# Kernel tuning notes

Measured on AMD Instinct MI355X. Metric: run time of the kernel, lower is better.

The kernel has to match this reference:

```python
import jax, jax.numpy as jnp
import numpy as np

B, R, S, M, L = 16, 64, 128, 64, 128  # batch, regions, src_dim, message_dim, max_latent
E = R * R - R  # 4032 directed edges (all ordered pairs, no self loops)


def _edge_indices():
    s, t = np.meshgrid(np.arange(R), np.arange(R), indexing='ij')
    mask = s != t
    return s[mask].astype(np.int64), t[mask].astype(np.int64)


def setup_inputs() -> dict:
    key = jax.random.key(0)
    ks = jax.random.split(key, 8)
    src_np, tgt_np = _edge_indices()
    xav_ms = float(np.sqrt(6.0 / (M + S)))  # xavier_uniform bound for (M,S) matrices
    small = 0.02  # torch inits add_w/gain_w to zeros; use small random for non-trivial outputs
    return {
        'source': jax.random.normal(ks[0], (B, R, S), jnp.float32),
        'mean_w': jax.random.uniform(ks[1], (E, M, S), jnp.float32, -xav_ms, xav_ms),
        'mean_b': jnp.zeros((E, M), jnp.float32),
        'logstd_w': jax.random.uniform(ks[2], (E, M, S), jnp.float32, -xav_ms, xav_ms),
        'logstd_b': jnp.zeros((E, M), jnp.float32),
        'add_w': small * jax.random.normal(ks[3], (E, L, M), jnp.float32),
        'gain_w': small * jax.random.normal(ks[4], (E, L, M), jnp.float32),
        'src_idx': jnp.asarray(src_np),
        'tgt_idx': jnp.asarray(tgt_np),
        'deterministic': 1,
    }


def reference(source, mean_w, mean_b, logstd_w, logstd_b, add_w, gain_w,
              src_idx, tgt_idx, deterministic):
    B_, E_ = source.shape[0], src_idx.shape[0]
    # gather source features per edge: [B, E, S]
    src = source[:, src_idx, :]
    # per-edge grouped GEMMs
    mean = jnp.einsum('bes,ems->bem', src, mean_w) + mean_b      # [B, E, M]
    logstd = jnp.einsum('bes,ems->bem', src, logstd_w) + logstd_b
    # deterministic path: msg = mean (softplus(std) only used when sampling)
    msg = mean
    add = jnp.einsum('bem,elm->bel', msg, add_w)                  # [B, E, L]
    gain = jnp.einsum('bem,elm->bel', msg, gain_w)
    # scatter-add over target regions
    inc_add = jnp.zeros((B_, R, L), source.dtype).at[:, tgt_idx].add(add)
    inc_gain = jnp.zeros((B_, R, L), source.dtype).at[:, tgt_idx].add(gain)
    # scatter (unique flat indices) into dense [B, R, R, M] message tensors
    flat = src_idx * R + tgt_idx
    def scat(x):
        return jnp.zeros((B_, R * R, M), source.dtype).at[:, flat].set(x).reshape(B_, R, R, M)
    return inc_add, inc_gain, scat(mean), scat(logstd), scat(msg)
```

## Files before the change

### kernel.cpp

```cpp
#include <hip/hip_runtime.h>

#define BB 16
#define RR 64
#define SS 128
#define MM 64
#define LL 128
#define EE 4032

#define OUT3_OFF 262144
#define ARR_SZ   4194304

__global__ __launch_bounds__(256) void k_zero(float* __restrict__ out) {
  int tid = blockIdx.x * 256 + threadIdx.x;
  if (tid < 262144) { out[tid] = 0.0f; return; }
  int idx = tid - 262144;
  int a = idx >> 16;
  int r = idx & 65535;
  int b = r >> 12;
  int d = (r >> 6) & 63;
  int m = r & 63;
  out[OUT3_OFF + (size_t)a * ARR_SZ + (size_t)b * 262144 + d * 4160 + m] = 0.0f;
}

__global__ __launch_bounds__(256) void k_edge(
    const float* __restrict__ source,
    const float* __restrict__ mean_w,
    const float* __restrict__ mean_b,
    const float* __restrict__ logstd_w,
    const float* __restrict__ logstd_b,
    const int* __restrict__ src_idx,
    const int* __restrict__ tgt_idx,
    float* __restrict__ out)
{
  __shared__ float lds_src[BB * 132];
  __shared__ float lds_mean[BB * 64];
  __shared__ float lds_logstd[BB * 64];
  const int e = blockIdx.x;
  const int tid = threadIdx.x;
  const int sidx = src_idx[e];
  const int tidx = tgt_idx[e];

  #pragma unroll
  for (int f0 = 0; f0 < 2; ++f0) {
    int f = tid + f0 * 256;
    int b = f >> 5, s4 = f & 31;
    float4 v = *(const float4*)(source + ((size_t)b * (RR * SS) + (size_t)sidx * SS + s4 * 4));
    *(float4*)(lds_src + b * 132 + s4 * 4) = v;
  }

  const int m = tid >> 2;
  const int sq = tid & 3;

  const float* wmp = mean_w   + ((size_t)e * (MM * SS) + (size_t)m * SS) + sq * 4;
  const float* wlp = logstd_w + ((size_t)e * (MM * SS) + (size_t)m * SS) + sq * 4;

  float4 a0 = *(const float4*)(wmp + 0);
  float4 c0 = *(const float4*)(wlp + 0);
  float4 a1 = *(const float4*)(wmp + 16);
  float4 c1 = *(const float4*)(wlp + 16);

  __syncthreads();

  float accm[BB], accl[BB];
  #pragma unroll
  for (int b = 0; b < BB; ++b) { accm[b] = 0.0f; accl[b] = 0.0f; }

  #pragma unroll
  for (int k = 0; k < 8; ++k) {
    float4 a2 = {}, c2 = {};
    if (k < 6) {
      a2 = *(const float4*)(wmp + (k + 2) * 16);
      c2 = *(const float4*)(wlp + (k + 2) * 16);
    }
    const int soff = sq * 4 + k * 16;
    #pragma unroll
    for (int b = 0; b < BB; ++b) {
      float4 sv = *(const float4*)(lds_src + b * 132 + soff);
      accm[b] = fmaf(a0.x, sv.x, fmaf(a0.y, sv.y, fmaf(a0.z, sv.z, fmaf(a0.w, sv.w, accm[b]))));
      accl[b] = fmaf(c0.x, sv.x, fmaf(c0.y, sv.y, fmaf(c0.z, sv.z, fmaf(c0.w, sv.w, accl[b]))));
    }
    a0 = a1; c0 = c1; a1 = a2; c1 = c2;
  }
  #pragma unroll
  for (int b = 0; b < BB; ++b) {
    accm[b] += __shfl_xor(accm[b], 1);
    accm[b] += __shfl_xor(accm[b], 2);
    accl[b] += __shfl_xor(accl[b], 1);
    accl[b] += __shfl_xor(accl[b], 2);
  }
  const float bm = mean_b[e * MM + m];
  const float bl = logstd_b[e * MM + m];
  #pragma unroll
  for (int j = 0; j < 4; ++j) {
    int b = sq * 4 + j;
    lds_mean[b * 64 + m]   = accm[b] + bm;
    lds_logstd[b * 64 + m] = accl[b] + bl;
  }
  __syncthreads();

  float* out3 = out + OUT3_OFF;
  float* out4 = out3 + ARR_SZ;
  float* out5 = out4 + ARR_SZ;
  const size_t rowbase = (size_t)(sidx * RR + tidx) * MM;
  const int b = tid >> 4, m4 = tid & 15;
  float4 vm = *(float4*)(lds_mean + b * 64 + m4 * 4);
  float4 vl = *(float4*)(lds_logstd + b * 64 + m4 * 4);
  size_t o = (size_t)b * (RR * RR * MM) + rowbase + m4 * 4;
  *(float4*)(out3 + o) = vm;
  *(float4*)(out4 + o) = vl;
  *(float4*)(out5 + o) = vm;
}

__global__ __launch_bounds__(256) void k_inc(
    const float* __restrict__ add_w,
    const float* __restrict__ gain_w,
    float* __restrict__ out)
{
  __shared__ float lds_mean[2][BB * 64];
  const int g = blockIdx.x;
  const int tt = g / 18;
  const int r = g % 18;
  const int lh = r / 9;
  const int c = r % 9;
  const int tid = threadIdx.x;
  const int l_loc = tid >> 2;
  const int mq = tid & 3;
  const int l = lh * 64 + l_loc;
  const int b16 = tid >> 4, m4 = tid & 15;

  const float* out3 = out + OUT3_OFF;

  float acca[BB], accg[BB];
  #pragma unroll
  for (int b = 0; b < BB; ++b) { acca[b] = 0.0f; accg[b] = 0.0f; }

  float4 mv_n;
  float4 wa_n[4], wg_n[4];
  {
    const int si = c * 7;
    const int s = si + (si >= tt ? 1 : 0);
    const int e = s * 63 + (tt > s ? tt - 1 : tt);
    mv_n = *(const float4*)(out3 + ((size_t)b16 * 262144 + (size_t)(s * 64 + tt) * 64 + m4 * 4));
    const float* wa = add_w  + ((size_t)e * (LL * MM) + (size_t)l * MM + mq * 16);
    const float* wg = gain_w + ((size_t)e * (LL * MM) + (size_t)l * MM + mq * 16);
    #pragma unroll
    for (int i = 0; i < 4; ++i) {
      wa_n[i] = *(const float4*)(wa + i * 4);
      wg_n[i] = *(const float4*)(wg + i * 4);
    }
  }

  #pragma unroll
  for (int j = 0; j < 7; ++j) {
    float4 mv = mv_n;
    float4 wa_c[4], wg_c[4];
    #pragma unroll
    for (int i = 0; i < 4; ++i) { wa_c[i] = wa_n[i]; wg_c[i] = wg_n[i]; }

    *(float4*)(&lds_mean[j & 1][b16 * 64 + m4 * 4]) = mv;
    __syncthreads();

    if (j < 6) {
      const int si2 = c * 7 + j + 1;
      const int s2 = si2 + (si2 >= tt ? 1 : 0);
      const int e2 = s2 * 63 + (tt > s2 ? tt - 1 : tt);
      mv_n = *(const float4*)(out3 + ((size_t)b16 * 262144 + (size_t)(s2 * 64 + tt) * 64 + m4 * 4));
      const float* wa2 = add_w  + ((size_t)e2 * (LL * MM) + (size_t)l * MM + mq * 16);
      const float* wg2 = gain_w + ((size_t)e2 * (LL * MM) + (size_t)l * MM + mq * 16);
      #pragma unroll
      for (int i = 0; i < 4; ++i) {
        wa_n[i] = *(const float4*)(wa2 + i * 4);
        wg_n[i] = *(const float4*)(wg2 + i * 4);
      }
    }

    #pragma unroll
    for (int i = 0; i < 4; ++i) {
      float4 a  = wa_c[i];
      float4 gq = wg_c[i];
      #pragma unroll
      for (int b = 0; b < BB; ++b) {
        float4 mvv = *(const float4*)(&lds_mean[j & 1][b * 64 + mq * 16 + i * 4]);
        acca[b] = fmaf(a.x,  mvv.x, fmaf(a.y,  mvv.y, fmaf(a.z,  mvv.z, fmaf(a.w,  mvv.w, acca[b]))));
        accg[b] = fmaf(gq.x, mvv.x, fmaf(gq.y, mvv.y, fmaf(gq.z, mvv.z, fmaf(gq.w, mvv.w, accg[b]))));
      }
    }
  }
  #pragma unroll
  for (int b = 0; b < BB; ++b) {
    acca[b] += __shfl_xor(acca[b], 1);
    acca[b] += __shfl_xor(acca[b], 2);
    accg[b] += __shfl_xor(accg[b], 1);
    accg[b] += __shfl_xor(accg[b], 2);
  }
  float* inc_add  = out;
  float* inc_gain = out + 131072;
  #pragma unroll
  for (int jj = 0; jj < 4; ++jj) {
    int b = mq * 4 + jj;
    size_t o = (size_t)b * (RR * LL) + (size_t)tt * LL + l;
    atomicAdd(inc_add + o, acca[b]);
    atomicAdd(inc_gain + o, accg[b]);
  }
}

extern "C" void kernel_launch(void* const* d_in, const int* in_sizes, int n_in,
                              void* d_out, int out_size, void* d_ws, size_t ws_size,
                              hipStream_t stream) {
  const float* source   = (const float*)d_in[0];
  const float* mean_w   = (const float*)d_in[1];
  const float* mean_b   = (const float*)d_in[2];
  const float* logstd_w = (const float*)d_in[3];
  const float* logstd_b = (const float*)d_in[4];
  const float* add_w    = (const float*)d_in[5];
  const float* gain_w   = (const float*)d_in[6];
  const int*   src_idx  = (const int*)d_in[7];
  const int*   tgt_idx  = (const int*)d_in[8];
  float* out = (float*)d_out;

  k_zero<<<1792, 256, 0, stream>>>(out);
  k_edge<<<EE, 256, 0, stream>>>(source, mean_w, mean_b, logstd_w, logstd_b,
                                 src_idx, tgt_idx, out);
  k_inc<<<1152, 256, 0, stream>>>(add_w, gain_w, out);
}
```

Before: 479.1 us.

## Stream edge weights into LDS via async global_load_lds with a ring buffer

The edge kernel now loads source rows and mean/logstd weight tiles straight from global memory into LDS with global_load_lds, using a four-slot ring buffer. Explicit vmcnt waits let compute on one k-chunk overlap the loads for later chunks. This removes the register staging for weights and aims to keep more memory requests in flight. In exchange it relies on manual waitcnt counting and the per-wave LDS layout being right, and it drops the padding on the source rows, which may add LDS bank conflicts.

```diff
diff --git a/kernel.cpp b/kernel.cpp
--- a/kernel.cpp
+++ b/kernel.cpp
@@ -9,6 +9,12 @@
 
 #define OUT3_OFF 262144
 #define ARR_SZ   4194304
+
+__device__ __forceinline__ void g2l16(const float* g, const float* l) {
+  __builtin_amdgcn_global_load_lds(
+      (const __attribute__((address_space(1))) unsigned int*)g,
+      (__attribute__((address_space(3))) unsigned int*)l, 16, 0, 0);
+}
 
 __global__ __launch_bounds__(256) void k_zero(float* __restrict__ out) {
   int tid = blockIdx.x * 256 + threadIdx.x;
@@ -32,55 +38,65 @@
     const int* __restrict__ tgt_idx,
     float* __restrict__ out)
 {
-  __shared__ float lds_src[BB * 132];
-  __shared__ float lds_mean[BB * 64];
-  __shared__ float lds_logstd[BB * 64];
+  __shared__ float lds[10240];
   const int e = blockIdx.x;
   const int tid = threadIdx.x;
+  const int w = tid >> 6, lane = tid & 63;
   const int sidx = src_idx[e];
   const int tidx = tgt_idx[e];
 
-  #pragma unroll
-  for (int f0 = 0; f0 < 2; ++f0) {
-    int f = tid + f0 * 256;
-    int b = f >> 5, s4 = f & 31;
-    float4 v = *(const float4*)(source + ((size_t)b * (RR * SS) + (size_t)sidx * SS + s4 * 4));
-    *(float4*)(lds_src + b * 132 + s4 * 4) = v;
-  }
-
-  const int m = tid >> 2;
-  const int sq = tid & 3;
-
-  const float* wmp = mean_w   + ((size_t)e * (MM * SS) + (size_t)m * SS) + sq * 4;
-  const float* wlp = logstd_w + ((size_t)e * (MM * SS) + (size_t)m * SS) + sq * 4;
-
-  float4 a0 = *(const float4*)(wmp + 0);
-  float4 c0 = *(const float4*)(wlp + 0);
-  float4 a1 = *(const float4*)(wmp + 16);
-  float4 c1 = *(const float4*)(wlp + 16);
-
-  __syncthreads();
+  {
+    int f0 = tid;
+    g2l16(source + (size_t)(f0 >> 5) * (RR * SS) + (size_t)sidx * SS + (f0 & 31) * 4,
+          lds + w * 256);
+    int f1 = tid + 256;
+    g2l16(source + (size_t)(f1 >> 5) * (RR * SS) + (size_t)sidx * SS + (f1 & 31) * 4,
+          lds + 1024 + w * 256);
+  }
+  __builtin_amdgcn_sched_barrier(0);
+
+  const int row = w * 16 + (lane >> 2);
+  const int sq4 = (lane & 3) * 4;
+  const float* wmg = mean_w   + (size_t)e * (MM * SS) + (size_t)row * SS + sq4;
+  const float* wlg = logstd_w + (size_t)e * (MM * SS) + (size_t)row * SS + sq4;
+  #pragma unroll
+  for (int kk = 0; kk < 4; ++kk) {
+    g2l16(wmg + kk * 16, lds + 2048 + kk * 1024 + w * 256);
+    g2l16(wlg + kk * 16, lds + 6144 + kk * 1024 + w * 256);
+  }
+  __builtin_amdgcn_sched_barrier(0);
+
+  asm volatile("s_waitcnt vmcnt(8)" ::: "memory");
+  __builtin_amdgcn_s_barrier();
 
   float accm[BB], accl[BB];
   #pragma unroll
   for (int b = 0; b < BB; ++b) { accm[b] = 0.0f; accl[b] = 0.0f; }
 
-  #pragma unroll
-  for (int k = 0; k < 8; ++k) {
-    float4 a2 = {}, c2 = {};
-    if (k < 6) {
-      a2 = *(const float4*)(wmp + (k + 2) * 16);
-      c2 = *(const float4*)(wlp + (k + 2) * 16);
-    }
-    const int soff = sq * 4 + k * 16;
-    #pragma unroll
-    for (int b = 0; b < BB; ++b) {
-      float4 sv = *(const float4*)(lds_src + b * 132 + soff);
-      accm[b] = fmaf(a0.x, sv.x, fmaf(a0.y, sv.y, fmaf(a0.z, sv.z, fmaf(a0.w, sv.w, accm[b]))));
-      accl[b] = fmaf(c0.x, sv.x, fmaf(c0.y, sv.y, fmaf(c0.z, sv.z, fmaf(c0.w, sv.w, accl[b]))));
-    }
-    a0 = a1; c0 = c1; a1 = a2; c1 = c2;
-  }
+#define KSTEP(kk, Nwait)                                                        \
+  {                                                                             \
+    asm volatile("s_waitcnt vmcnt(" #Nwait ")" ::: "memory");                   \
+    float4 a = *(const float4*)(lds + 2048 + ((kk) & 3) * 1024 + w * 256 + lane * 4); \
+    float4 c = *(const float4*)(lds + 6144 + ((kk) & 3) * 1024 + w * 256 + lane * 4); \
+    const int soff = sq4 + (kk) * 16;                                           \
+    _Pragma("unroll")                                                           \
+    for (int b = 0; b < BB; ++b) {                                              \
+      float4 sv = *(const float4*)(lds + b * 128 + soff);                       \
+      accm[b] = fmaf(a.x, sv.x, fmaf(a.y, sv.y, fmaf(a.z, sv.z, fmaf(a.w, sv.w, accm[b])))); \
+      accl[b] = fmaf(c.x, sv.x, fmaf(c.y, sv.y, fmaf(c.z, sv.z, fmaf(c.w, sv.w, accl[b])))); \
+    }                                                                           \
+    if ((kk) < 4) {                                                             \
+      __builtin_amdgcn_sched_barrier(0);    \
+      g2l16(wmg + ((kk) + 4) * 16, lds + 2048 + (kk) * 1024 + w * 256);         \
+      g2l16(wlg + ((kk) + 4) * 16, lds + 6144 + (kk) * 1024 + w * 256);         \
+      __builtin_amdgcn_sched_barrier(0);                                        \
+    }                                                                           \
+  }
+
+  KSTEP(0, 6) KSTEP(1, 6) KSTEP(2, 6) KSTEP(3, 6)
+  KSTEP(4, 6) KSTEP(5, 4) KSTEP(6, 2) KSTEP(7, 0)
+#undef KSTEP
+
   #pragma unroll
   for (int b = 0; b < BB; ++b) {
     accm[b] += __shfl_xor(accm[b], 1);
@@ -88,13 +104,17 @@
     accl[b] += __shfl_xor(accl[b], 1);
     accl[b] += __shfl_xor(accl[b], 2);
   }
+  const int m = tid >> 2;
+  const int sq = tid & 3;
   const float bm = mean_b[e * MM + m];
   const float bl = logstd_b[e * MM + m];
+
+  __syncthreads();
   #pragma unroll
   for (int j = 0; j < 4; ++j) {
     int b = sq * 4 + j;
-    lds_mean[b * 64 + m]   = accm[b] + bm;
-    lds_logstd[b * 64 + m] = accl[b] + bl;
+    lds[b * 64 + m]        = accm[b] + bm;
+    lds[1024 + b * 64 + m] = accl[b] + bl;
   }
   __syncthreads();
 
@@ -102,10 +122,10 @@
   float* out4 = out3 + ARR_SZ;
   float* out5 = out4 + ARR_SZ;
   const size_t rowbase = (size_t)(sidx * RR + tidx) * MM;
-  const int b = tid >> 4, m4 = tid & 15;
-  float4 vm = *(float4*)(lds_mean + b * 64 + m4 * 4);
-  float4 vl = *(float4*)(lds_logstd + b * 64 + m4 * 4);
-  size_t o = (size_t)b * (RR * RR * MM) + rowbase + m4 * 4;
+  const int b16 = tid >> 4, m4 = tid & 15;
+  float4 vm = *(float4*)(lds + b16 * 64 + m4 * 4);
+  float4 vl = *(float4*)(lds + 1024 + b16 * 64 + m4 * 4);
+  size_t o = (size_t)b16 * (RR * RR * MM) + rowbase + m4 * 4;
   *(float4*)(out3 + o) = vm;
   *(float4*)(out4 + o) = vl;
   *(float4*)(out5 + o) = vm;
```

New measurement: 483.6 us. About the same (+0.9%).
